# Kernel optimization log

Hardware: AMD Instinct MI355X
Metric: run time of the kernel (lower is better)

## Reference

```python
import jax, jax.numpy as jnp
import numpy as np

N, D_IN, D_OUT = 8192, 512, 512


def setup_inputs() -> dict:
    key = jax.random.key(0)
    ks = jax.random.split(key, 8)
    scale_in = 1.0 / np.sqrt(D_IN)
    scale_cat = 1.0 / np.sqrt(2 * D_OUT)
    return {
        "x": jax.random.normal(ks[0], (N, D_IN), dtype=jnp.float32),
        "adj": jax.random.randint(ks[1], (N, N), 0, 2, dtype=jnp.int32),
        "W_self": jax.random.uniform(ks[2], (D_IN, D_OUT), jnp.float32, -scale_in, scale_in),
        "b_self": jax.random.uniform(ks[3], (D_OUT,), jnp.float32, -scale_in, scale_in),
        "W_nb": jax.random.uniform(ks[4], (D_IN, D_OUT), jnp.float32, -scale_in, scale_in),
        "b_nb": jax.random.uniform(ks[5], (D_OUT,), jnp.float32, -scale_in, scale_in),
        "W_comb": jax.random.uniform(ks[6], (2 * D_OUT, D_OUT), jnp.float32, -scale_cat, scale_cat),
        "b_comb": jax.random.uniform(ks[7], (D_OUT,), jnp.float32, -scale_cat, scale_cat),
    }


def reference(x, adj, W_self, b_self, W_nb, b_nb, W_comb, b_comb):
    # Vectorized equivalent of the per-node loop:
    # neighbors_i = where(adj[i] > 0); agg_i = mean(x[neighbors_i]) (zeros if none)
    mask = (adj > 0).astype(x.dtype)              # [N, N]
    deg = jnp.sum(mask, axis=1, keepdims=True)    # [N, 1]
    # sum over neighbors is mask @ x; dividing by max(deg,1) yields zeros when deg==0
    agg = (mask @ x) / jnp.maximum(deg, 1.0)      # [N, D_IN]
    self_f = x @ W_self + b_self                  # [N, D_OUT]
    nb_f = agg @ W_nb + b_nb                      # [N, D_OUT]
    combined = jnp.concatenate([self_f, nb_f], axis=-1)  # [N, 2*D_OUT]
    out = combined @ W_comb + b_comb              # [N, D_OUT]
    return jax.nn.relu(out)
```

## Files before the change

kernel.cpp:

```cpp
#include <hip/hip_runtime.h>


using short8 = __attribute__((ext_vector_type(8))) short;
using f32x4  = __attribute__((ext_vector_type(4))) float;
using f32x16 = __attribute__((ext_vector_type(16))) float;

typedef unsigned short U16;
typedef unsigned int   U32;
typedef unsigned long long U64;

__device__ __forceinline__ U16 f2bf(float f) {
  U32 u = __float_as_uint(f);
  u = (u + 0x7fffu + ((u >> 16) & 1u)) >> 16;
  return (U16)u;
}
__device__ __forceinline__ U32 pack2bf(float a, float b) {
  return (U32)f2bf(a) | ((U32)f2bf(b) << 16);
}
__device__ __forceinline__ U32 exp2bits(U32 w, int j) {
  U32 t2 = (w >> (2 * j)) & 3u;
  return ((t2 | (t2 << 15)) & 0x10001u) * 0x3F80u;
}

__global__ __launch_bounds__(256, 2)
void GraphSAGELayer_773094114149_kernel(
    int phase,
    const float* __restrict__ x,     const int* __restrict__ adj,
    const float* __restrict__ Wself, const float* __restrict__ bself,
    const float* __restrict__ Wnb,   const float* __restrict__ bnb,
    const float* __restrict__ Wcomb, const float* __restrict__ bcomb,
    U16* __restrict__ xTt, U16* __restrict__ aggp, U64* __restrict__ bits,
    float* __restrict__ invdeg, U16* __restrict__ Wt,
    float* __restrict__ cbias, float* __restrict__ outp)
{
  extern __shared__ __align__(16) unsigned char smem[];
  const int tid = threadIdx.x;

  if (phase == 0) {
    if (blockIdx.x < 256) {
      const int n0 = blockIdx.x * 2;
      float* red = (float*)smem;
      float s0 = 0.f, s1 = 0.f;
#pragma unroll
      for (int jj = 0; jj < 4; ++jj) {
        int j = tid * 4 + jj;
        float bvv = (j < 512) ? bself[j] : bnb[j - 512];
        s0 += bvv * Wcomb[(size_t)j * 512 + n0];
        s1 += bvv * Wcomb[(size_t)j * 512 + n0 + 1];
      }
      red[tid] = s0; red[256 + tid] = s1;
      __syncthreads();
      for (int st = 128; st > 0; st >>= 1) {
        if (tid < st) {
          red[tid]       += red[tid + st];
          red[256 + tid] += red[256 + tid + st];
        }
        __syncthreads();
      }
      if (tid == 0) {
        cbias[n0]     = red[0]   + bcomb[n0];
        cbias[n0 + 1] = red[256] + bcomb[n0 + 1];
      }
      return;
    }
    if (blockIdx.x < 768) {
      const int b2   = blockIdx.x - 256;
      const int half = b2 >> 8;
      const int k0   = (b2 & 255) * 2;
      const float* Wsrc = half ? Wnb : Wself;
      const int woff = half * 512;
      float* wsf = (float*)smem;
      {
        int idx = tid * 4;
        *(float4*)&wsf[idx] = *(const float4*)&Wsrc[(size_t)(k0 + (idx >> 9)) * 512 + (idx & 511)];
      }
      __syncthreads();
      float a00 = 0.f, a01 = 0.f, a10 = 0.f, a11 = 0.f;
#pragma unroll 8
      for (int j = 0; j < 512; ++j) {
        float wc0 = Wcomb[(size_t)(woff + j) * 512 + tid];
        float wc1 = Wcomb[(size_t)(woff + j) * 512 + tid + 256];
        float s0 = wsf[j], s1 = wsf[512 + j];
        a00 += s0 * wc0;  a01 += s0 * wc1;
        a10 += s1 * wc0;  a11 += s1 * wc1;
      }
      Wt[(size_t)tid * 1024 + woff + k0]             = f2bf(a00);
      Wt[(size_t)tid * 1024 + woff + k0 + 1]         = f2bf(a10);
      Wt[(size_t)(tid + 256) * 1024 + woff + k0]     = f2bf(a01);
      Wt[(size_t)(tid + 256) * 1024 + woff + k0 + 1] = f2bf(a11);
      return;
    }
    if (blockIdx.x < 1792) {
      const int b = blockIdx.x - 768;
      const int n0 = (b & 7) * 64;
      const int m0 = (b >> 3) * 64;
      U16* tl = (U16*)smem;
      const int r  = tid >> 2;
      const int cq = (tid & 3) * 16;
      const float* src = x + (size_t)(m0 + r) * 512 + n0 + cq;
      U32 pk[8];
#pragma unroll
      for (int i = 0; i < 8; ++i) {
        float2 f = *(const float2*)(src + 2 * i);
        pk[i] = pack2bf(f.x, f.y);
      }
#pragma unroll
      for (int i = 0; i < 8; ++i) {
        tl[(cq + 2*i)     * 72 + r] = (U16)(pk[i] & 0xffffu);
        tl[(cq + 2*i + 1) * 72 + r] = (U16)(pk[i] >> 16);
      }
      __syncthreads();
      const int c2 = tid >> 2;
      const int mq = (tid & 3) * 16;
      uint4 o0 = *(const uint4*)&tl[c2 * 72 + mq];
      uint4 o1 = *(const uint4*)&tl[c2 * 72 + mq + 8];
      const int tile  = n0 >> 6;
      const int obase = (m0 + mq) >> 3;
      U16* d = xTt + (((size_t)tile * 1024 + obase) * 64 + c2) * 8;
      *(uint4*)d         = o0;
      *(uint4*)(d + 512) = o1;
      return;
    }
    {
      const int row = blockIdx.x - 1792;
      const int wv = tid >> 6, ln = tid & 63;
      const int* arow = adj + (size_t)row * 8192 + wv * 2048;
      U64* brow = bits + (size_t)row * 128 + wv * 32;
      float* sdeg = (float*)smem;
      int v[32];
#pragma unroll
      for (int p = 0; p < 32; ++p) v[p] = arow[p * 64 + ln];
      int dsum = 0;
#pragma unroll
      for (int p = 0; p < 32; ++p) {
        U64 mask = __ballot(v[p] > 0);
        dsum += (int)__popcll(mask);
        if (ln == 0) brow[p] = mask;
      }
      if (ln == 0) sdeg[wv] = (float)dsum;
      __syncthreads();
      if (tid == 0)
        invdeg[row] = 1.0f / fmaxf(sdeg[0] + sdeg[1] + sdeg[2] + sdeg[3], 1.0f);
      return;
    }
  }

  const int lane = tid & 63;
  const int wave = tid >> 6;

  if (phase == 1) {
    U16* Aa = (U16*)smem;
    const U64* bits64 = (const U64*)bits;
    const int wr = wave & 1;
    const int wc = wave >> 1;
    const int mBase = blockIdx.y * 128;

    const int r = tid >> 1, h = tid & 1;
    const U64* abase = bits64 + (size_t)(mBase + r) * 128 + h;
    U16* awr = Aa + r * 128;
    const int rx = r & 15;

    const U16* bbase = xTt + (size_t)blockIdx.x * 524288;
    const int bni = ((wc * 32 + (lane & 31)) + (lane >> 5) * 64) * 8;

    f32x16 acc[2];
#pragma unroll
    for (int a = 0; a < 2; ++a)
#pragma unroll
      for (int i = 0; i < 16; ++i) acc[a][i] = 0.f;

    U64 ab = abase[0], abn = 0;
    uint4 bv[8], bn[8];
#pragma unroll
    for (int ks = 0; ks < 8; ++ks)
      bv[ks] = *(const uint4*)(bbase + bni + ks * 1024);
#pragma unroll
    for (int ks = 0; ks < 8; ++ks) bn[ks] = bv[ks];

    for (int it = 0; it < 64; ++it) {
      __syncthreads();

      {
        U32 wlo = (U32)ab, whi = (U32)(ab >> 32);
        U32 o[32];
#pragma unroll
        for (int j = 0; j < 16; ++j) {
          o[j]      = exp2bits(wlo, j);
          o[16 + j] = exp2bits(whi, j);
        }
#pragma unroll
        for (int i = 0; i < 8; ++i)
          *(uint4*)(awr + (((h * 8 + i) ^ rx) * 8)) =
              make_uint4(o[4*i], o[4*i+1], o[4*i+2], o[4*i+3]);
      }

      __syncthreads();

      if (it + 1 < 64) {
        abn = abase[(it + 1) * 2];
#pragma unroll
        for (int ks = 0; ks < 8; ++ks)
          bn[ks] = *(const uint4*)(bbase + bni + ((it + 1) * 16 + ks * 2) * 512);
      }

#pragma unroll
      for (int ks = 0; ks < 8; ++ks) {
        const int ko = ks * 2 + (lane >> 5);
        short8 bf = *(short8*)&bv[ks];
#pragma unroll
        for (int tm = 0; tm < 2; ++tm) {
          int m = wr * 64 + tm * 32 + (lane & 31);
          short8 af = *(const short8*)(Aa + m * 128 + ((ko ^ (m & 15)) * 8));
          acc[tm] = __builtin_amdgcn_mfma_f32_32x32x16_bf16(af, bf, acc[tm], 0, 0, 0);
        }
      }

      ab = abn;
#pragma unroll
      for (int ks = 0; ks < 8; ++ks) bv[ks] = bn[ks];
    }

    const int col = blockIdx.x * 64 + wc * 32 + (lane & 31);
#pragma unroll
    for (int tm = 0; tm < 2; ++tm) {
      const int rbase = mBase + wr * 64 + tm * 32 + 4 * (lane >> 5);
#pragma unroll
      for (int i = 0; i < 16; ++i) {
        int row = rbase + (i & 3) + 8 * (i >> 2);
        aggp[(size_t)row * 512 + col] = f2bf(acc[tm][i] * invdeg[row]);
      }
    }
    return;
  }

  {
    U16* As2 = (U16*)smem;
    U16* Bs2 = (U16*)(smem + 8192);
    const int quad = lane >> 4;
    const int wm = (wave & 1) * 32;
    const int wn = (wave >> 1) * 64;
    const int nBase = blockIdx.x * 128;
    const int mBase = blockIdx.y * 64;

    int amr[2], agc[2]; U16* alp[2];
#pragma unroll
    for (int i = 0; i < 2; ++i) {
      int c  = i * 256 + tid;
      amr[i] = c >> 3;
      agc[i] = c & 7;
      alp[i] = As2 + amr[i] * 64 + ((agc[i] ^ (amr[i] & 7)) * 8);
    }
    const U16* bgp[4]; U16* blp[4];
#pragma unroll
    for (int i = 0; i < 4; ++i) {
      int c  = i * 256 + tid;
      int nr = c >> 3;
      int gc = c & 7;
      bgp[i] = Wt + (size_t)(nBase + nr) * 1024 + gc * 8;
      blp[i] = Bs2 + nr * 64 + ((gc ^ (nr & 7)) * 8);
    }

    f32x4 acc[2][4];
#pragma unroll
    for (int a = 0; a < 2; ++a)
#pragma unroll
      for (int b = 0; b < 4; ++b) acc[a][b] = (f32x4){0.f, 0.f, 0.f, 0.f};

    uint4 av[2], bv[4];
#pragma unroll
    for (int i = 0; i < 2; ++i) {
      const float* ap = x + (size_t)(mBase + amr[i]) * 512 + agc[i] * 8;
      float4 f0 = *(const float4*)ap;
      float4 f1 = *(const float4*)(ap + 4);
      av[i] = make_uint4(pack2bf(f0.x,f0.y), pack2bf(f0.z,f0.w),
                         pack2bf(f1.x,f1.y), pack2bf(f1.z,f1.w));
    }
#pragma unroll
    for (int i = 0; i < 4; ++i) bv[i] = *(const uint4*)(bgp[i]);

    for (int it = 0; it < 16; ++it) {
      __syncthreads();
#pragma unroll
      for (int i = 0; i < 2; ++i) *(uint4*)alp[i] = av[i];
#pragma unroll
      for (int i = 0; i < 4; ++i) *(uint4*)blp[i] = bv[i];
      __syncthreads();

      if (it + 1 < 16) {
        const int it1 = it + 1;
        if (it1 < 8) {
#pragma unroll
          for (int i = 0; i < 2; ++i) {
            const float* ap = x + (size_t)(mBase + amr[i]) * 512 + it1 * 64 + agc[i] * 8;
            float4 f0 = *(const float4*)ap;
            float4 f1 = *(const float4*)(ap + 4);
            av[i] = make_uint4(pack2bf(f0.x,f0.y), pack2bf(f0.z,f0.w),
                               pack2bf(f1.x,f1.y), pack2bf(f1.z,f1.w));
          }
        } else {
#pragma unroll
          for (int i = 0; i < 2; ++i)
            av[i] = *(const uint4*)(aggp + (size_t)(mBase + amr[i]) * 512 +
                                    (it1 - 8) * 64 + agc[i] * 8);
        }
#pragma unroll
        for (int i = 0; i < 4; ++i) bv[i] = *(const uint4*)(bgp[i] + it1 * 64);
      }

#pragma unroll
      for (int s = 0; s < 2; ++s) {
        short8 af[2], bfr[4];
        const int g = s * 4 + quad;
#pragma unroll
        for (int tm = 0; tm < 2; ++tm) {
          int m = wm + tm * 16 + (lane & 15);
          af[tm] = *(const short8*)(As2 + m * 64 + ((g ^ (m & 7)) * 8));
        }
#pragma unroll
        for (int tn = 0; tn < 4; ++tn) {
          int n = wn + tn * 16 + (lane & 15);
          bfr[tn] = *(const short8*)(Bs2 + n * 64 + ((g ^ (n & 7)) * 8));
        }
#pragma unroll
        for (int tm = 0; tm < 2; ++tm)
#pragma unroll
          for (int tn = 0; tn < 4; ++tn)
            acc[tm][tn] = __builtin_amdgcn_mfma_f32_16x16x32_bf16(
                af[tm], bfr[tn], acc[tm][tn], 0, 0, 0);
      }
    }

    float bias[4];
#pragma unroll
    for (int tn = 0; tn < 4; ++tn)
      bias[tn] = cbias[nBase + wn + tn * 16 + (lane & 15)];

#pragma unroll
    for (int tm = 0; tm < 2; ++tm) {
      int rb = wm + tm * 16 + quad * 4;
#pragma unroll
      for (int tn = 0; tn < 4; ++tn) {
        int n = nBase + wn + tn * 16 + (lane & 15);
#pragma unroll
        for (int rr = 0; rr < 4; ++rr) {
          float v = fmaxf(acc[tm][tn][rr] + bias[tn], 0.0f);
          outp[(size_t)(mBase + rb + rr) * 512 + n] = v;
        }
      }
    }
  }
}

extern "C" void kernel_launch(void* const* d_in, const int* in_sizes, int n_in,
                              void* d_out, int out_size, void* d_ws, size_t ws_size,
                              hipStream_t stream) {
  (void)in_sizes; (void)n_in; (void)out_size; (void)ws_size;

  const float* x     = (const float*)d_in[0];
  const int*   adj   = (const int*)d_in[1];
  const float* Wself = (const float*)d_in[2];
  const float* bself = (const float*)d_in[3];
  const float* Wnb   = (const float*)d_in[4];
  const float* bnb   = (const float*)d_in[5];
  const float* Wcomb = (const float*)d_in[6];
  const float* bcomb = (const float*)d_in[7];
  float* out = (float*)d_out;

  char* ws = (char*)d_ws;
  U16*   xTt    = (U16*)(ws);
  U16*   aggp   = (U16*)(ws + 8388608);
  U64*   bits   = (U64*)(ws + 16777216);
  U16*   Wt     = (U16*)(ws + 25165824);
  float* cbias  = (float*)(ws + 26214400);
  float* invdeg = (float*)(ws + 26216448);

#define ARGS(P) (P), x, adj, Wself, bself, Wnb, bnb, Wcomb, bcomb, \
                xTt, aggp, bits, invdeg, Wt, cbias, out
  GraphSAGELayer_773094114149_kernel<<<dim3(9984),   256,  9216, stream>>>(ARGS(0));
  GraphSAGELayer_773094114149_kernel<<<dim3(8, 64),  256, 32768, stream>>>(ARGS(1));
  GraphSAGELayer_773094114149_kernel<<<dim3(4, 128), 256, 24576, stream>>>(ARGS(2));
#undef ARGS
}
```

Before: 532.3 us.

## Double-buffer adjacency tile in LDS and vectorize adjacency bit-packing

```diff
diff --git a/kernel.cpp b/kernel.cpp
--- a/kernel.cpp
+++ b/kernel.cpp
@@ -20,6 +20,19 @@
 __device__ __forceinline__ U32 exp2bits(U32 w, int j) {
   U32 t2 = (w >> (2 * j)) & 3u;
   return ((t2 | (t2 << 15)) & 0x10001u) * 0x3F80u;
+}
+__device__ __forceinline__ void unpackA(U64 ab, U16* awr, int h, int rx) {
+  U32 wlo = (U32)ab, whi = (U32)(ab >> 32);
+  U32 o[32];
+#pragma unroll
+  for (int j = 0; j < 16; ++j) {
+    o[j]      = exp2bits(wlo, j);
+    o[16 + j] = exp2bits(whi, j);
+  }
+#pragma unroll
+  for (int i = 0; i < 8; ++i)
+    *(uint4*)(awr + (((h * 8 + i) ^ rx) * 8)) =
+        make_uint4(o[4*i], o[4*i+1], o[4*i+2], o[4*i+3]);
 }
 
 __global__ __launch_bounds__(256, 2)
@@ -123,24 +136,28 @@
     }
     {
       const int row = blockIdx.x - 1792;
-      const int wv = tid >> 6, ln = tid & 63;
-      const int* arow = adj + (size_t)row * 8192 + wv * 2048;
-      U64* brow = bits + (size_t)row * 128 + wv * 32;
-      float* sdeg = (float*)smem;
-      int v[32];
-#pragma unroll
-      for (int p = 0; p < 32; ++p) v[p] = arow[p * 64 + ln];
-      int dsum = 0;
-#pragma unroll
-      for (int p = 0; p < 32; ++p) {
-        U64 mask = __ballot(v[p] > 0);
-        dsum += (int)__popcll(mask);
-        if (ln == 0) brow[p] = mask;
-      }
-      if (ln == 0) sdeg[wv] = (float)dsum;
+      const int* base = adj + (size_t)row * 8192 + tid * 32;
+      int4 v[8];
+#pragma unroll
+      for (int i = 0; i < 8; ++i) v[i] = ((const int4*)base)[i];
+      U32 w = 0;
+#pragma unroll
+      for (int i = 0; i < 8; ++i) {
+        w |= (U32)(v[i].x > 0) << (4 * i);
+        w |= (U32)(v[i].y > 0) << (4 * i + 1);
+        w |= (U32)(v[i].z > 0) << (4 * i + 2);
+        w |= (U32)(v[i].w > 0) << (4 * i + 3);
+      }
+      ((U32*)bits)[(size_t)row * 256 + tid] = w;
+
+      int dsum = __popc(w);
+#pragma unroll
+      for (int off = 32; off > 0; off >>= 1) dsum += __shfl_down(dsum, off);
+      int* sred = (int*)smem;
+      if ((tid & 63) == 0) sred[tid >> 6] = dsum;
       __syncthreads();
       if (tid == 0)
-        invdeg[row] = 1.0f / fmaxf(sdeg[0] + sdeg[1] + sdeg[2] + sdeg[3], 1.0f);
+        invdeg[row] = 1.0f / fmaxf((float)(sred[0] + sred[1] + sred[2] + sred[3]), 1.0f);
       return;
     }
   }
@@ -149,7 +166,8 @@
   const int wave = tid >> 6;
 
   if (phase == 1) {
-    U16* Aa = (U16*)smem;
+    U16* Abuf0 = (U16*)smem;
+    U16* Abuf1 = (U16*)(smem + 32768);
     const U64* bits64 = (const U64*)bits;
     const int wr = wave & 1;
     const int wc = wave >> 1;
@@ -157,7 +175,7 @@
 
     const int r = tid >> 1, h = tid & 1;
     const U64* abase = bits64 + (size_t)(mBase + r) * 128 + h;
-    U16* awr = Aa + r * 128;
+    const int awroff = r * 128;
     const int rx = r & 15;
 
     const U16* bbase = xTt + (size_t)blockIdx.x * 524288;
@@ -169,38 +187,27 @@
 #pragma unroll
       for (int i = 0; i < 16; ++i) acc[a][i] = 0.f;
 
-    U64 ab = abase[0], abn = 0;
-    uint4 bv[8], bn[8];
+    U64 ab0 = abase[0];
+    uint4 bv[8];
 #pragma unroll
     for (int ks = 0; ks < 8; ++ks)
       bv[ks] = *(const uint4*)(bbase + bni + ks * 1024);
-#pragma unroll
-    for (int ks = 0; ks < 8; ++ks) bn[ks] = bv[ks];
+    unpackA(ab0, Abuf0 + awroff, h, rx);
+    U64 abn = abase[2];
+    __syncthreads();
 
     for (int it = 0; it < 64; ++it) {
-      __syncthreads();
-
-      {
-        U32 wlo = (U32)ab, whi = (U32)(ab >> 32);
-        U32 o[32];
-#pragma unroll
-        for (int j = 0; j < 16; ++j) {
-          o[j]      = exp2bits(wlo, j);
-          o[16 + j] = exp2bits(whi, j);
-        }
-#pragma unroll
-        for (int i = 0; i < 8; ++i)
-          *(uint4*)(awr + (((h * 8 + i) ^ rx) * 8)) =
-              make_uint4(o[4*i], o[4*i+1], o[4*i+2], o[4*i+3]);
-      }
-
-      __syncthreads();
-
+      U16* curA = (it & 1) ? Abuf1 : Abuf0;
+      U16* nxtA = (it & 1) ? Abuf0 : Abuf1;
+
+      if (it + 1 < 64) unpackA(abn, nxtA + awroff, h, rx);
+
+      uint4 bn[8];
       if (it + 1 < 64) {
-        abn = abase[(it + 1) * 2];
 #pragma unroll
         for (int ks = 0; ks < 8; ++ks)
           bn[ks] = *(const uint4*)(bbase + bni + ((it + 1) * 16 + ks * 2) * 512);
+        if (it + 2 < 64) abn = abase[(it + 2) * 2];
       }
 
 #pragma unroll
@@ -210,14 +217,14 @@
 #pragma unroll
         for (int tm = 0; tm < 2; ++tm) {
           int m = wr * 64 + tm * 32 + (lane & 31);
-          short8 af = *(const short8*)(Aa + m * 128 + ((ko ^ (m & 15)) * 8));
+          short8 af = *(const short8*)(curA + m * 128 + ((ko ^ (m & 15)) * 8));
           acc[tm] = __builtin_amdgcn_mfma_f32_32x32x16_bf16(af, bf, acc[tm], 0, 0, 0);
         }
       }
 
-      ab = abn;
 #pragma unroll
       for (int ks = 0; ks < 8; ++ks) bv[ks] = bn[ks];
+      __syncthreads();
     }
 
     const int col = blockIdx.x * 64 + wc * 32 + (lane & 31);
@@ -377,7 +384,7 @@
 #define ARGS(P) (P), x, adj, Wself, bself, Wnb, bnb, Wcomb, bcomb, \
                 xTt, aggp, bits, invdeg, Wt, cbias, out
   GraphSAGELayer_773094114149_kernel<<<dim3(9984),   256,  9216, stream>>>(ARGS(0));
-  GraphSAGELayer_773094114149_kernel<<<dim3(8, 64),  256, 32768, stream>>>(ARGS(1));
+  GraphSAGELayer_773094114149_kernel<<<dim3(8, 64),  256, 65536, stream>>>(ARGS(1));
   GraphSAGELayer_773094114149_kernel<<<dim3(4, 128), 256, 24576, stream>>>(ARGS(2));
 #undef ARGS
 }
```

After: 535.4 us. About the same (+0.6%).
